# Performance work log

Measured on AMD Instinct MI355X. Metric: run time of the kernel, lower is better.

## Reference

```python
import jax, jax.numpy as jnp
import numpy as np

EMBED_DIM = 1024
NUM_HEADS = 16
HEAD_DIM = EMBED_DIM // NUM_HEADS


def setup_inputs() -> dict:
    key = jax.random.key(0)
    ks = jax.random.split(key, 9)
    B, T, C = 4, 2048, EMBED_DIM
    s = 1.0 / np.sqrt(C)
    return {
        "x": jax.random.normal(ks[0], (B, T, C), jnp.float32),
        "Wq": jax.random.normal(ks[1], (C, C), jnp.float32) * s,
        "bq": jnp.zeros((C,), jnp.float32),
        "Wk": jax.random.normal(ks[2], (C, C), jnp.float32) * s,
        "bk": jnp.zeros((C,), jnp.float32),
        "Wv": jax.random.normal(ks[3], (C, C), jnp.float32) * s,
        "bv": jnp.zeros((C,), jnp.float32),
        "Wo": jax.random.normal(ks[4], (C, C), jnp.float32) * s,
        "bo": jnp.zeros((C,), jnp.float32),
    }


def reference(x, Wq, bq, Wk, bk, Wv, bv, Wo, bo):
    B, T, C = x.shape
    H, D = NUM_HEADS, HEAD_DIM
    # projections (torch Linear: y = x @ W.T + b; here weights stored as [in, out])
    q = (x @ Wq + bq).reshape(B, T, H, D).transpose(0, 2, 1, 3)  # [B,H,T,D]
    k = (x @ Wk + bk).reshape(B, T, H, D).transpose(0, 2, 1, 3)
    v = (x @ Wv + bv).reshape(B, T, H, D).transpose(0, 2, 1, 3)
    scores = jnp.einsum("bhqd,bhkd->bhqk", q, k) / jnp.sqrt(jnp.float32(D))
    causal = jnp.tril(jnp.ones((T, T), bool))
    scores = jnp.where(causal, scores, -jnp.inf)
    attn = jax.nn.softmax(scores, axis=-1)
    out = jnp.einsum("bhqk,bhkd->bhqd", attn, v)  # [B,H,T,D]
    out = out.transpose(0, 2, 1, 3).reshape(B, T, C)
    return out @ Wo + bo
```

## Files before the change

kernel.cpp:

```cpp
#include <hip/hip_runtime.h>
#include <hip/hip_bf16.h>
#include <math.h>

typedef __hip_bfloat16 bf16_t;
typedef __attribute__((ext_vector_type(8))) short short8;
typedef __attribute__((ext_vector_type(4))) float floatx4;

#define T_SEQ 2048
#define NB    4
#define NH    16
#define HD    64
#define C_DIM 1024
#define M_ROWS (NB * T_SEQ)

#define Q_SCALE 0.18033688011f

__device__ __forceinline__ void load_lds16(const bf16_t* g, bf16_t* l) {
    __builtin_amdgcn_global_load_lds(
        (const __attribute__((address_space(1))) void*)g,
        (__attribute__((address_space(3))) void*)l,
        16, 0, 0);
}

__device__ __forceinline__ floatx4 mfma16(short8 a, short8 b, floatx4 c) {
    return __builtin_amdgcn_mfma_f32_16x16x32_bf16(a, b, c, 0, 0, 0);
}

__global__ void convert_x_kernel(const float* __restrict__ x, bf16_t* __restrict__ xb) {
    int i = blockIdx.x * 256 + threadIdx.x;
    float4 v = reinterpret_cast<const float4*>(x)[i];
    union { bf16_t h[4]; short4 s4; } u;
    u.h[0] = __float2bfloat16(v.x);
    u.h[1] = __float2bfloat16(v.y);
    u.h[2] = __float2bfloat16(v.z);
    u.h[3] = __float2bfloat16(v.w);
    reinterpret_cast<short4*>(xb)[i] = u.s4;
}

__global__ void transpose_cvt_kernel(const float* __restrict__ W0, const float* __restrict__ W1,
                                     const float* __restrict__ W2, const float* __restrict__ W3,
                                     bf16_t* __restrict__ O0, bf16_t* __restrict__ O1,
                                     bf16_t* __restrict__ O2, bf16_t* __restrict__ O3) {
    const float* W = (blockIdx.z == 0) ? W0 : (blockIdx.z == 1) ? W1 : (blockIdx.z == 2) ? W2 : W3;
    bf16_t*      O = (blockIdx.z == 0) ? O0 : (blockIdx.z == 1) ? O1 : (blockIdx.z == 2) ? O2 : O3;
    __shared__ float tile[32][33];
    int bx = blockIdx.x * 32, by = blockIdx.y * 32;
    int tx = threadIdx.x, ty = threadIdx.y;
#pragma unroll
    for (int j = 0; j < 32; j += 8)
        tile[ty + j][tx] = W[(size_t)(by + ty + j) * C_DIM + bx + tx];
    __syncthreads();
#pragma unroll
    for (int j = 0; j < 32; j += 8)
        O[(size_t)(bx + ty + j) * C_DIM + by + tx] = __float2bfloat16(tile[tx][ty + j]);
}

__device__ __forceinline__ void gemm_mainloop(const bf16_t* __restrict__ Ablk,
                                              const bf16_t* __restrict__ Bblk,
                                              bf16_t* As, bf16_t* Bs,
                                              floatx4 acc[4][4], int wave, int lane) {
    int lr = lane & 15, lq = lane >> 4;
    int wr = (wave >> 1) * 64, wc = (wave & 1) * 64;
    for (int kt = 0; kt < C_DIM; kt += 64) {
#pragma unroll
        for (int j = 0; j < 4; ++j) {
            int chunk = j * 256 + wave * 64 + lane;
            int r = chunk >> 3, ps = chunk & 7;
            int c = ((ps ^ (r & 7)) * 8);
            load_lds16(Ablk + (size_t)r * C_DIM + kt + c, As + chunk * 8);
            load_lds16(Bblk + (size_t)r * C_DIM + kt + c, Bs + chunk * 8);
        }
        __syncthreads();
#pragma unroll
        for (int kk = 0; kk < 2; ++kk) {
            short8 af[4], bfr[4];
            int psw = ((kk * 4 + lq) ^ (lr & 7)) * 8;
#pragma unroll
            for (int m = 0; m < 4; ++m)
                af[m] = *reinterpret_cast<const short8*>(As + (wr + m * 16 + lr) * 64 + psw);
#pragma unroll
            for (int n = 0; n < 4; ++n)
                bfr[n] = *reinterpret_cast<const short8*>(Bs + (wc + n * 16 + lr) * 64 + psw);
#pragma unroll
            for (int m = 0; m < 4; ++m)
#pragma unroll
                for (int n = 0; n < 4; ++n)
                    acc[m][n] = mfma16(af[m], bfr[n], acc[m][n]);
        }
        __syncthreads();
    }
}

__global__ __launch_bounds__(256, 3) void gemm_qkv_kernel(
    const bf16_t* __restrict__ xb,
    const bf16_t* __restrict__ WqT, const bf16_t* __restrict__ WkT, const bf16_t* __restrict__ WvT,
    const float* __restrict__ bq, const float* __restrict__ bk, const float* __restrict__ bv,
    bf16_t* __restrict__ Q, bf16_t* __restrict__ K, bf16_t* __restrict__ Vt) {
    __shared__ bf16_t As[128 * 64];
    __shared__ bf16_t Bs[128 * 64];
    int tid = threadIdx.x, wave = tid >> 6, lane = tid & 63;

    int f    = (int)blockIdx.x + ((int)blockIdx.y << 3) + ((int)blockIdx.z << 9);
    int xcd  = f & 7;
    int s    = f >> 3;
    int rloc = s & 7;
    int t2   = s >> 3;
    int colp = t2 & 7;
    int wsel = t2 >> 3;
    int row0 = (xcd * 8 + rloc) * 128;
    int col0 = colp * 128;

    const bf16_t* Wt  = (wsel == 0) ? WqT : (wsel == 1) ? WkT : WvT;
    const float* bias = (wsel == 0) ? bq : (wsel == 1) ? bk : bv;

    floatx4 acc[4][4] = {};
    gemm_mainloop(xb + (size_t)row0 * C_DIM, Wt + (size_t)col0 * C_DIM, As, Bs, acc, wave, lane);

    int lr = lane & 15, lq = lane >> 4;
    int wr = (wave >> 1) * 64, wc = (wave & 1) * 64;

    if (wsel == 2) {
#pragma unroll
        for (int nt = 0; nt < 4; ++nt) {
            int col = col0 + wc + nt * 16 + lr;
            float bvv = bias[col];
            int h = col >> 6, d = col & 63;
#pragma unroll
            for (int m = 0; m < 4; ++m) {
                int rowg0 = row0 + wr + m * 16 + lq * 4;
                int b = rowg0 >> 11, t0 = rowg0 & (T_SEQ - 1);
                union { bf16_t h4[4]; short4 s4; } u;
#pragma unroll
                for (int r = 0; r < 4; ++r)
                    u.h4[r] = __float2bfloat16(acc[m][nt][r] + bvv);
                *reinterpret_cast<short4*>(
                    &Vt[((size_t)((b * NH + h) * HD + d)) * T_SEQ + t0]) = u.s4;
            }
        }
    } else {
        float scale = (wsel == 0) ? Q_SCALE : 1.0f;
        bf16_t* outp = (wsel == 0) ? Q : K;
#pragma unroll
        for (int nt = 0; nt < 4; ++nt) {
            int col = col0 + wc + nt * 16 + lr;
            float bvv = bias[col];
            int h = col >> 6, d = col & 63;
#pragma unroll
            for (int m = 0; m < 4; ++m) {
#pragma unroll
                for (int r = 0; r < 4; ++r) {
                    int rowg = row0 + wr + m * 16 + lq * 4 + r;
                    int b = rowg >> 11, t = rowg & (T_SEQ - 1);
                    float val = (acc[m][nt][r] + bvv) * scale;
                    outp[((size_t)((b * NH + h) * T_SEQ + t)) * HD + d] =
                        __float2bfloat16(val);
                }
            }
        }
    }
}

__global__ __launch_bounds__(256, 2) void attn_kernel(
    const bf16_t* __restrict__ Q, const bf16_t* __restrict__ K,
    const bf16_t* __restrict__ Vt, bf16_t* __restrict__ ctx) {
    __shared__ __align__(16) bf16_t Ks[2][128 * 64];
    __shared__ __align__(16) bf16_t Vs[2][64 * 128];
    int tid = threadIdx.x, w = tid >> 6, lane = tid & 63;
    int lr = lane & 15, lq = lane >> 4;
    int xcd = (int)blockIdx.x;
    int y   = (int)blockIdx.y;
    int bh  = xcd * 8 + (y & 7);
    int qp  = y >> 3;
    int b = bh >> 4, h = bh & 15;

    const bf16_t* Kbase = K  + (size_t)bh * T_SEQ * HD;
    const bf16_t* Vbase = Vt + (size_t)bh * HD * T_SEQ;

    int buf = 0;
#pragma unroll 1
    for (int pass = 0; pass < 2; ++pass) {
        int qt = pass ? qp : (15 - qp);
        int q0 = qt * 128;
        int ktiles = qt + 1;
        const bf16_t* Qbase = Q + ((size_t)bh * T_SEQ + q0) * HD;

        {
            int kt0s = 0;
#pragma unroll
            for (int cc = 0; cc < 4; ++cc) {
                int ch = tid + cc * 256;
                int r = ch >> 3, ps = ch & 7;
                int c = (ps ^ (r & 7)) * 8;
                load_lds16(Kbase + (size_t)(kt0s + r) * HD + c, Ks[buf] + ch * 8);
                int rv = ch >> 4, pv = ch & 15;
                int cv = (pv ^ (rv & 7)) * 8;
                load_lds16(Vbase + (size_t)rv * T_SEQ + kt0s + cv, Vs[buf] + ch * 8);
            }
        }

        short8 qf[2][2];
#pragma unroll
        for (int g = 0; g < 2; ++g)
#pragma unroll
            for (int kk = 0; kk < 2; ++kk)
                qf[g][kk] = *reinterpret_cast<const short8*>(
                    Qbase + (size_t)(w * 32 + g * 16 + lr) * HD + kk * 32 + lq * 8);

        floatx4 o[2][4] = {};
        float lpart[2] = {0.f, 0.f};

        for (int it = 0; it < ktiles; ++it) {
            __syncthreads();

            if (it + 1 < ktiles) {
                int nk0 = (it + 1) * 128;
#pragma unroll
                for (int cc = 0; cc < 4; ++cc) {
                    int ch = tid + cc * 256;
                    int r = ch >> 3, ps = ch & 7;
                    int c = (ps ^ (r & 7)) * 8;
                    load_lds16(Kbase + (size_t)(nk0 + r) * HD + c, Ks[buf ^ 1] + ch * 8);
                    int rv = ch >> 4, pv = ch & 15;
                    int cv = (pv ^ (rv & 7)) * 8;
                    load_lds16(Vbase + (size_t)rv * T_SEQ + nk0 + cv, Vs[buf ^ 1] + ch * 8);
                }
            }

            const bf16_t* Kc = Ks[buf];
            const bf16_t* Vc = Vs[buf];
            bool last = (it == ktiles - 1);

#pragma unroll
            for (int sub = 0; sub < 2; ++sub) {
                int ktb = it * 128 + sub * 64;

                floatx4 s[2][4] = {};
                {
                    short8 kf[4][2];
#pragma unroll
                    for (int kk = 0; kk < 2; ++kk) {
                        int psw = ((kk * 4 + lq) ^ (lr & 7)) * 8;
#pragma unroll
                        for (int n = 0; n < 4; ++n)
                            kf[n][kk] = *reinterpret_cast<const short8*>(
                                Kc + (sub * 64 + n * 16 + lr) * 64 + psw);
                    }
#pragma unroll
                    for (int g = 0; g < 2; ++g)
#pragma unroll
                        for (int kk = 0; kk < 2; ++kk)
#pragma unroll
                            for (int n = 0; n < 4; ++n)
                                s[g][n] = mfma16(kf[n][kk], qf[g][kk], s[g][n]);
                }

                if (last) {
#pragma unroll
                    for (int g = 0; g < 2; ++g) {
                        int rowg = q0 + w * 32 + g * 16 + lr;
#pragma unroll
                        for (int n = 0; n < 4; ++n)
#pragma unroll
                            for (int r = 0; r < 4; ++r) {
                                int colg = ktb + n * 16 + lq * 4 + r;
                                if (colg > rowg) s[g][n][r] = -1e30f;
                            }
                    }
                }

                short8 pf[2][2];
#pragma unroll
                for (int g = 0; g < 2; ++g) {
#pragma unroll
                    for (int n = 0; n < 4; ++n)
#pragma unroll
                        for (int r = 0; r < 4; ++r)
                            s[g][n][r] = __builtin_amdgcn_exp2f(s[g][n][r]);
                    float p0 = (s[g][0][0] + s[g][0][1]) + (s[g][0][2] + s[g][0][3]);
                    float p1 = (s[g][1][0] + s[g][1][1]) + (s[g][1][2] + s[g][1][3]);
                    float p2 = (s[g][2][0] + s[g][2][1]) + (s[g][2][2] + s[g][2][3]);
                    float p3 = (s[g][3][0] + s[g][3][1]) + (s[g][3][2] + s[g][3][3]);
                    lpart[g] += (p0 + p1) + (p2 + p3);

                    unsigned upk[4][2];
#pragma unroll
                    for (int n = 0; n < 4; ++n) {
                        asm("v_cvt_pk_bf16_f32 %0, %1, %2"
                            : "=v"(upk[n][0]) : "v"(s[g][n][0]), "v"(s[g][n][1]));
                        asm("v_cvt_pk_bf16_f32 %0, %1, %2"
                            : "=v"(upk[n][1]) : "v"(s[g][n][2]), "v"(s[g][n][3]));
                    }
#pragma unroll
                    for (int kk = 0; kk < 2; ++kk) {
                        unsigned x0 = upk[2 * kk][0], y0 = upk[2 * kk + 1][0];
                        unsigned x1 = upk[2 * kk][1], y1 = upk[2 * kk + 1][1];
                        asm("v_permlane32_swap_b32 %0, %1" : "+v"(x0), "+v"(y0));
                        asm("v_permlane32_swap_b32 %0, %1" : "+v"(x1), "+v"(y1));
                        asm("v_permlane16_swap_b32 %0, %1" : "+v"(x0), "+v"(y0));
                        asm("v_permlane16_swap_b32 %0, %1" : "+v"(x1), "+v"(y1));
                        union { unsigned u4[4]; short8 s8; } pk;
                        pk.u4[0] = x0; pk.u4[1] = x1; pk.u4[2] = y0; pk.u4[3] = y1;
                        pf[g][kk] = pk.s8;
                    }
                }

                short8 vf[4][2];
#pragma unroll
                for (int kk = 0; kk < 2; ++kk) {
                    int psw = ((sub * 8 + kk * 4 + lq) ^ (lr & 7)) * 8;
#pragma unroll
                    for (int dt = 0; dt < 4; ++dt)
                        vf[dt][kk] = *reinterpret_cast<const short8*>(
                            Vc + (dt * 16 + lr) * 128 + psw);
                }
#pragma unroll
                for (int g = 0; g < 2; ++g)
#pragma unroll
                    for (int kk = 0; kk < 2; ++kk)
#pragma unroll
                        for (int dt = 0; dt < 4; ++dt)
                            o[g][dt] = mfma16(pf[g][kk], vf[dt][kk], o[g][dt]);
            }

            buf ^= 1;
        }

#pragma unroll
        for (int g = 0; g < 2; ++g) {
            float l = lpart[g];
            l += __shfl_xor(l, 16);
            l += __shfl_xor(l, 32);
            float inv = 1.0f / l;
#pragma unroll
            for (int r = 0; r < 4; ++r) {
                float invr = __shfl(inv, (lane & 48) | (lq * 4 + r));
                int t = q0 + w * 32 + g * 16 + lq * 4 + r;
#pragma unroll
                for (int dt = 0; dt < 4; ++dt) {
                    int d = dt * 16 + lr;
                    ctx[((size_t)(b * T_SEQ + t)) * C_DIM + h * HD + d] =
                        __float2bfloat16(o[g][dt][r] * invr);
                }
            }
        }
    }
}

__global__ __launch_bounds__(256, 3) void gemm_out_kernel(
    const bf16_t* __restrict__ Actx, const bf16_t* __restrict__ WoT,
    const float* __restrict__ bo, float* __restrict__ out) {
    __shared__ bf16_t As[128 * 64];
    __shared__ bf16_t Bs[128 * 64];
    int tid = threadIdx.x, wave = tid >> 6, lane = tid & 63;

    int f    = (int)blockIdx.x + ((int)blockIdx.y << 3);
    int xcd  = f & 7;
    int s    = f >> 3;
    int rloc = s & 7;
    int colp = s >> 3;
    int row0 = (xcd * 8 + rloc) * 128;
    int col0 = colp * 128;

    floatx4 acc[4][4] = {};
    gemm_mainloop(Actx + (size_t)row0 * C_DIM, WoT + (size_t)col0 * C_DIM, As, Bs, acc, wave, lane);
    int lr = lane & 15, lq = lane >> 4;
    int wr = (wave >> 1) * 64, wc = (wave & 1) * 64;
#pragma unroll
    for (int nt = 0; nt < 4; ++nt) {
        int col = col0 + wc + nt * 16 + lr;
        float bvv = bo[col];
#pragma unroll
        for (int m = 0; m < 4; ++m)
#pragma unroll
            for (int r = 0; r < 4; ++r) {
                int rowg = row0 + wr + m * 16 + lq * 4 + r;
                out[(size_t)rowg * C_DIM + col] = acc[m][nt][r] + bvv;
            }
    }
}

extern "C" void kernel_launch(void* const* d_in, const int* in_sizes, int n_in,
                              void* d_out, int out_size, void* d_ws, size_t ws_size,
                              hipStream_t stream) {
    const float* x  = (const float*)d_in[0];
    const float* Wq = (const float*)d_in[1];
    const float* bq = (const float*)d_in[2];
    const float* Wk = (const float*)d_in[3];
    const float* bk = (const float*)d_in[4];
    const float* Wv = (const float*)d_in[5];
    const float* bv = (const float*)d_in[6];
    const float* Wo = (const float*)d_in[7];
    const float* bo = (const float*)d_in[8];
    float* out = (float*)d_out;

    char* ws = (char*)d_ws;
    bf16_t* xb  = (bf16_t*)ws; ws += (size_t)M_ROWS * C_DIM * 2;
    bf16_t* WqT = (bf16_t*)ws; ws += (size_t)C_DIM * C_DIM * 2;
    bf16_t* WkT = (bf16_t*)ws; ws += (size_t)C_DIM * C_DIM * 2;
    bf16_t* WvT = (bf16_t*)ws; ws += (size_t)C_DIM * C_DIM * 2;
    bf16_t* WoT = (bf16_t*)ws; ws += (size_t)C_DIM * C_DIM * 2;
    bf16_t* Qb  = (bf16_t*)ws; ws += (size_t)M_ROWS * C_DIM * 2;
    bf16_t* Kb  = (bf16_t*)ws; ws += (size_t)M_ROWS * C_DIM * 2;
    bf16_t* Vtb = (bf16_t*)ws; ws += (size_t)M_ROWS * C_DIM * 2;
    bf16_t* ctx = (bf16_t*)ws; ws += (size_t)M_ROWS * C_DIM * 2;

    convert_x_kernel<<<(M_ROWS * C_DIM / 4) / 256, 256, 0, stream>>>(x, xb);
    transpose_cvt_kernel<<<dim3(32, 32, 4), dim3(32, 8), 0, stream>>>(
        Wq, Wk, Wv, Wo, WqT, WkT, WvT, WoT);
    gemm_qkv_kernel<<<dim3(8, 64, 3), 256, 0, stream>>>(
        xb, WqT, WkT, WvT, bq, bk, bv, Qb, Kb, Vtb);
    attn_kernel<<<dim3(8, 64), 256, 0, stream>>>(Qb, Kb, Vtb, ctx);
    gemm_out_kernel<<<dim3(8, 64), 256, 0, stream>>>(ctx, WoT, bo, out);
}
```

Baseline: 230.9 us.

## Interleave two attention sub-tiles, skip fully masked half, raise MFMA priority

The attention inner loop no longer processes its two 64-key sub-tiles one after the other. QK^T for both halves is issued before the softmax of the first half, so exp and pack work can overlap with matrix ops. On the diagonal tile, waves 0-1 skip the second half entirely, since all of its keys lie beyond their rows. s_setprio is raised around the MFMA bursts to favour matrix issue across waves. The cost is higher register pressure from holding both score sets and the V fragments at once.

```diff
diff --git a/kernel.cpp b/kernel.cpp
--- a/kernel.cpp
+++ b/kernel.cpp
@@ -185,16 +185,15 @@
         const bf16_t* Qbase = Q + ((size_t)bh * T_SEQ + q0) * HD;
 
         {
-            int kt0s = 0;
 #pragma unroll
             for (int cc = 0; cc < 4; ++cc) {
                 int ch = tid + cc * 256;
                 int r = ch >> 3, ps = ch & 7;
                 int c = (ps ^ (r & 7)) * 8;
-                load_lds16(Kbase + (size_t)(kt0s + r) * HD + c, Ks[buf] + ch * 8);
+                load_lds16(Kbase + (size_t)r * HD + c, Ks[buf] + ch * 8);
                 int rv = ch >> 4, pv = ch & 15;
                 int cv = (pv ^ (rv & 7)) * 8;
-                load_lds16(Vbase + (size_t)rv * T_SEQ + kt0s + cv, Vs[buf] + ch * 8);
+                load_lds16(Vbase + (size_t)rv * T_SEQ + cv, Vs[buf] + ch * 8);
             }
         }
 
@@ -228,67 +227,96 @@
 
             const bf16_t* Kc = Ks[buf];
             const bf16_t* Vc = Vs[buf];
-            bool last = (it == ktiles - 1);
-
-#pragma unroll
-            for (int sub = 0; sub < 2; ++sub) {
-                int ktb = it * 128 + sub * 64;
-
-                floatx4 s[2][4] = {};
-                {
-                    short8 kf[4][2];
-#pragma unroll
-                    for (int kk = 0; kk < 2; ++kk) {
-                        int psw = ((kk * 4 + lq) ^ (lr & 7)) * 8;
+            bool last  = (it == ktiles - 1);
+            bool skip1 = last && (w < 2);
+
+            floatx4 s0[2][4] = {};
+            {
+                short8 kf[4][2];
+#pragma unroll
+                for (int kk = 0; kk < 2; ++kk) {
+                    int psw = ((kk * 4 + lq) ^ (lr & 7)) * 8;
+#pragma unroll
+                    for (int n = 0; n < 4; ++n)
+                        kf[n][kk] = *reinterpret_cast<const short8*>(
+                            Kc + (n * 16 + lr) * 64 + psw);
+                }
+                __builtin_amdgcn_s_setprio(1);
+#pragma unroll
+                for (int g = 0; g < 2; ++g)
+#pragma unroll
+                    for (int kk = 0; kk < 2; ++kk)
 #pragma unroll
                         for (int n = 0; n < 4; ++n)
-                            kf[n][kk] = *reinterpret_cast<const short8*>(
-                                Kc + (sub * 64 + n * 16 + lr) * 64 + psw);
-                    }
-#pragma unroll
-                    for (int g = 0; g < 2; ++g)
-#pragma unroll
-                        for (int kk = 0; kk < 2; ++kk)
-#pragma unroll
-                            for (int n = 0; n < 4; ++n)
-                                s[g][n] = mfma16(kf[n][kk], qf[g][kk], s[g][n]);
-                }
-
-                if (last) {
-#pragma unroll
-                    for (int g = 0; g < 2; ++g) {
+                            s0[g][n] = mfma16(kf[n][kk], qf[g][kk], s0[g][n]);
+                __builtin_amdgcn_s_setprio(0);
+            }
+
+            short8 vf0[4][2];
+#pragma unroll
+            for (int kk = 0; kk < 2; ++kk) {
+                int psw = ((kk * 4 + lq) ^ (lr & 7)) * 8;
+#pragma unroll
+                for (int dt = 0; dt < 4; ++dt)
+                    vf0[dt][kk] = *reinterpret_cast<const short8*>(
+                        Vc + (dt * 16 + lr) * 128 + psw);
+            }
+
+            floatx4 s1[2][4] = {};
+            if (!skip1) {
+                short8 kf[4][2];
+#pragma unroll
+                for (int kk = 0; kk < 2; ++kk) {
+                    int psw = ((kk * 4 + lq) ^ (lr & 7)) * 8;
+#pragma unroll
+                    for (int n = 0; n < 4; ++n)
+                        kf[n][kk] = *reinterpret_cast<const short8*>(
+                            Kc + (64 + n * 16 + lr) * 64 + psw);
+                }
+                __builtin_amdgcn_s_setprio(1);
+#pragma unroll
+                for (int g = 0; g < 2; ++g)
+#pragma unroll
+                    for (int kk = 0; kk < 2; ++kk)
+#pragma unroll
+                        for (int n = 0; n < 4; ++n)
+                            s1[g][n] = mfma16(kf[n][kk], qf[g][kk], s1[g][n]);
+                __builtin_amdgcn_s_setprio(0);
+            }
+
+            short8 pf0[2][2];
+            {
+                int ktb = it * 128;
+#pragma unroll
+                for (int g = 0; g < 2; ++g) {
+                    if (last) {
                         int rowg = q0 + w * 32 + g * 16 + lr;
 #pragma unroll
                         for (int n = 0; n < 4; ++n)
 #pragma unroll
                             for (int r = 0; r < 4; ++r) {
                                 int colg = ktb + n * 16 + lq * 4 + r;
-                                if (colg > rowg) s[g][n][r] = -1e30f;
+                                if (colg > rowg) s0[g][n][r] = -1e30f;
                             }
                     }
-                }
-
-                short8 pf[2][2];
-#pragma unroll
-                for (int g = 0; g < 2; ++g) {
 #pragma unroll
                     for (int n = 0; n < 4; ++n)
 #pragma unroll
                         for (int r = 0; r < 4; ++r)
-                            s[g][n][r] = __builtin_amdgcn_exp2f(s[g][n][r]);
-                    float p0 = (s[g][0][0] + s[g][0][1]) + (s[g][0][2] + s[g][0][3]);
-                    float p1 = (s[g][1][0] + s[g][1][1]) + (s[g][1][2] + s[g][1][3]);
-                    float p2 = (s[g][2][0] + s[g][2][1]) + (s[g][2][2] + s[g][2][3]);
-                    float p3 = (s[g][3][0] + s[g][3][1]) + (s[g][3][2] + s[g][3][3]);
+                            s0[g][n][r] = __builtin_amdgcn_exp2f(s0[g][n][r]);
+                    float p0 = (s0[g][0][0] + s0[g][0][1]) + (s0[g][0][2] + s0[g][0][3]);
+                    float p1 = (s0[g][1][0] + s0[g][1][1]) + (s0[g][1][2] + s0[g][1][3]);
+                    float p2 = (s0[g][2][0] + s0[g][2][1]) + (s0[g][2][2] + s0[g][2][3]);
+                    float p3 = (s0[g][3][0] + s0[g][3][1]) + (s0[g][3][2] + s0[g][3][3]);
                     lpart[g] += (p0 + p1) + (p2 + p3);
 
                     unsigned upk[4][2];
 #pragma unroll
                     for (int n = 0; n < 4; ++n) {
                         asm("v_cvt_pk_bf16_f32 %0, %1, %2"
-                            : "=v"(upk[n][0]) : "v"(s[g][n][0]), "v"(s[g][n][1]));
+                            : "=v"(upk[n][0]) : "v"(s0[g][n][0]), "v"(s0[g][n][1]));
                         asm("v_cvt_pk_bf16_f32 %0, %1, %2"
-                            : "=v"(upk[n][1]) : "v"(s[g][n][2]), "v"(s[g][n][3]));
+                            : "=v"(upk[n][1]) : "v"(s0[g][n][2]), "v"(s0[g][n][3]));
                     }
 #pragma unroll
                     for (int kk = 0; kk < 2; ++kk) {
@@ -300,26 +328,86 @@
                         asm("v_permlane16_swap_b32 %0, %1" : "+v"(x1), "+v"(y1));
                         union { unsigned u4[4]; short8 s8; } pk;
                         pk.u4[0] = x0; pk.u4[1] = x1; pk.u4[2] = y0; pk.u4[3] = y1;
-                        pf[g][kk] = pk.s8;
+                        pf0[g][kk] = pk.s8;
                     }
                 }
-
-                short8 vf[4][2];
+            }
+
+            __builtin_amdgcn_s_setprio(1);
+#pragma unroll
+            for (int g = 0; g < 2; ++g)
+#pragma unroll
+                for (int kk = 0; kk < 2; ++kk)
+#pragma unroll
+                    for (int dt = 0; dt < 4; ++dt)
+                        o[g][dt] = mfma16(pf0[g][kk], vf0[dt][kk], o[g][dt]);
+            __builtin_amdgcn_s_setprio(0);
+
+            if (!skip1) {
+                short8 vf1[4][2];
 #pragma unroll
                 for (int kk = 0; kk < 2; ++kk) {
-                    int psw = ((sub * 8 + kk * 4 + lq) ^ (lr & 7)) * 8;
+                    int psw = ((8 + kk * 4 + lq) ^ (lr & 7)) * 8;
 #pragma unroll
                     for (int dt = 0; dt < 4; ++dt)
-                        vf[dt][kk] = *reinterpret_cast<const short8*>(
+                        vf1[dt][kk] = *reinterpret_cast<const short8*>(
                             Vc + (dt * 16 + lr) * 128 + psw);
                 }
+                short8 pf1[2][2];
+                int ktb = it * 128 + 64;
+#pragma unroll
+                for (int g = 0; g < 2; ++g) {
+                    if (last) {
+                        int rowg = q0 + w * 32 + g * 16 + lr;
+#pragma unroll
+                        for (int n = 0; n < 4; ++n)
+#pragma unroll
+                            for (int r = 0; r < 4; ++r) {
+                                int colg = ktb + n * 16 + lq * 4 + r;
+                                if (colg > rowg) s1[g][n][r] = -1e30f;
+                            }
+                    }
+#pragma unroll
+                    for (int n = 0; n < 4; ++n)
+#pragma unroll
+                        for (int r = 0; r < 4; ++r)
+                            s1[g][n][r] = __builtin_amdgcn_exp2f(s1[g][n][r]);
+                    float p0 = (s1[g][0][0] + s1[g][0][1]) + (s1[g][0][2] + s1[g][0][3]);
+                    float p1 = (s1[g][1][0] + s1[g][1][1]) + (s1[g][1][2] + s1[g][1][3]);
+                    float p2 = (s1[g][2][0] + s1[g][2][1]) + (s1[g][2][2] + s1[g][2][3]);
+                    float p3 = (s1[g][3][0] + s1[g][3][1]) + (s1[g][3][2] + s1[g][3][3]);
+                    lpart[g] += (p0 + p1) + (p2 + p3);
+
+                    unsigned upk[4][2];
+#pragma unroll
+                    for (int n = 0; n < 4; ++n) {
+                        asm("v_cvt_pk_bf16_f32 %0, %1, %2"
+                            : "=v"(upk[n][0]) : "v"(s1[g][n][0]), "v"(s1[g][n][1]));
+                        asm("v_cvt_pk_bf16_f32 %0, %1, %2"
+                            : "=v"(upk[n][1]) : "v"(s1[g][n][2]), "v"(s1[g][n][3]));
+                    }
+#pragma unroll
+                    for (int kk = 0; kk < 2; ++kk) {
+                        unsigned x0 = upk[2 * kk][0], y0 = upk[2 * kk + 1][0];
+                        unsigned x1 = upk[2 * kk][1], y1 = upk[2 * kk + 1][1];
+                        asm("v_permlane32_swap_b32 %0, %1" : "+v"(x0), "+v"(y0));
+                        asm("v_permlane32_swap_b32 %0, %1" : "+v"(x1), "+v"(y1));
+                        asm("v_permlane16_swap_b32 %0, %1" : "+v"(x0), "+v"(y0));
+                        asm("v_permlane16_swap_b32 %0, %1" : "+v"(x1), "+v"(y1));
+                        union { unsigned u4[4]; short8 s8; } pk;
+                        pk.u4[0] = x0; pk.u4[1] = x1; pk.u4[2] = y0; pk.u4[3] = y1;
+                        pf1[g][kk] = pk.s8;
+                    }
+                }
+                __builtin_amdgcn_s_setprio(1);
 #pragma unroll
                 for (int g = 0; g < 2; ++g)
 #pragma unroll
                     for (int kk = 0; kk < 2; ++kk)
 #pragma unroll
                         for (int dt = 0; dt < 4; ++dt)
-                            o[g][dt] = mfma16(pf[g][kk], vf[dt][kk], o[g][dt]);
+                            o[g][dt] = mfma16(pf1[g][kk], vf1[dt][kk], o[g][dt]);
+                __builtin_amdgcn_s_setprio(0);
             }
 
             buf ^= 1;
```

After: 233.2 us. No clear change (+1.0%).
